# Performance work log

Hardware: AMD Instinct MI355X
Metric: run time of the kernel (lower is better)

Reference implementation:

```python
import jax, jax.numpy as jnp
import numpy as np

B, L, D = 2, 2048, 2048
H, HKV, HD = 32, 8, 64
G = H // HKV  # GQA group size


def _rope(t, cos, sin):
    # t: [B, h, L, HD]; cos/sin: [L, HD//2]; pairs are consecutive (view_as_complex)
    tr, ti = t[..., 0::2], t[..., 1::2]
    out_r = tr * cos - ti * sin
    out_i = tr * sin + ti * cos
    return jnp.stack([out_r, out_i], axis=-1).reshape(t.shape)


def setup_inputs() -> dict:
    key = jax.random.key(0)
    ks = jax.random.split(key, 5)
    x = jax.random.normal(ks[0], (B, L, D), dtype=jnp.float32)
    wq = jax.random.normal(ks[1], (D, H * HD), dtype=jnp.float32) * 0.02
    wk = jax.random.normal(ks[2], (D, HKV * HD), dtype=jnp.float32) * 0.02
    wv = jax.random.normal(ks[3], (D, HKV * HD), dtype=jnp.float32) * 0.02
    wo = jax.random.normal(ks[4], (D, D), dtype=jnp.float32) * 0.02
    # RoPE freqs: theta_i = 10000^(-2i/HD), angle[p, i] = p * theta_i
    inv_freq = 1.0 / (10000.0 ** (jnp.arange(0, HD, 2, dtype=jnp.float32) / HD))
    angles = jnp.arange(L, dtype=jnp.float32)[:, None] * inv_freq[None, :]  # [L, HD//2]
    freqs_cos = jnp.cos(angles)
    freqs_sin = jnp.sin(angles)
    # additive causal mask [L, L]
    mask = jnp.where(jnp.tril(jnp.ones((L, L), dtype=bool)), 0.0, -1e9).astype(jnp.float32)
    return {"x": x, "wq": wq, "wk": wk, "wv": wv, "wo": wo,
            "freqs_cos": freqs_cos, "freqs_sin": freqs_sin, "mask": mask}


def reference(x, wq, wk, wv, wo, freqs_cos, freqs_sin, mask):
    b, l, _ = x.shape
    q = (x @ wq).reshape(b, l, H, HD).transpose(0, 2, 1, 3)      # [B, H, L, HD]
    k = (x @ wk).reshape(b, l, HKV, HD).transpose(0, 2, 1, 3)    # [B, HKV, L, HD]
    v = (x @ wv).reshape(b, l, HKV, HD).transpose(0, 2, 1, 3)
    q = _rope(q, freqs_cos, freqs_sin)
    k = _rope(k, freqs_cos, freqs_sin)
    # native GQA broadcast instead of repeat_kv copy (same math)
    qg = q.reshape(b, HKV, G, l, HD)
    scores = jnp.einsum("bhgqd,bhkd->bhgqk", qg, k) / jnp.sqrt(jnp.float32(HD))
    scores = scores + mask  # [B, HKV, G, L, L]
    probs = jax.nn.softmax(scores.astype(jnp.float32), axis=-1).astype(v.dtype)
    out = jnp.einsum("bhgqk,bhkd->bhgqd", probs, v)              # [B, HKV, G, L, HD]
    out = out.reshape(b, H, l, HD).transpose(0, 2, 1, 3).reshape(b, l, H * HD)
    return out @ wo
```

## Files before the change

### kernel.cpp

```cpp
#include <hip/hip_runtime.h>
#include <hip/hip_bf16.h>

#define B_   2
#define L_   2048
#define D_   2048
#define H_   32
#define HKV_ 8
#define HD_  64
#define G_   4
#define M_   4096
#define NF_  3072

typedef __attribute__((ext_vector_type(8))) short bf16x8;
typedef __attribute__((ext_vector_type(4))) float f32x4;

static __device__ __forceinline__ unsigned short f2bf(float f) {
  unsigned int u = __float_as_uint(f);
  unsigned int r = (u + 0x7FFFu + ((u >> 16) & 1u)) >> 16;
  return (unsigned short)r;
}

#define GLD16(g, l) __builtin_amdgcn_global_load_lds(                      \
    (const __attribute__((address_space(1))) void*)(g),                    \
    (__attribute__((address_space(3))) void*)(l), 16, 0, 0)

__global__ void cast_bf16_kernel(const float* __restrict__ in,
                                 unsigned short* __restrict__ out, int n4) {
  int i = blockIdx.x * blockDim.x + threadIdx.x;
  if (i >= n4) return;
  float4 v = ((const float4*)in)[i];
  uint2 r;
  r.x = (unsigned int)f2bf(v.x) | ((unsigned int)f2bf(v.y) << 16);
  r.y = (unsigned int)f2bf(v.z) | ((unsigned int)f2bf(v.w) << 16);
  ((uint2*)out)[i] = r;
}

__global__ void transpose_cast_kernel(const float* __restrict__ src,
                                      unsigned short* __restrict__ dst,
                                      int K, int N) {
  __shared__ float tile[32][33];
  int k0 = blockIdx.y * 32, n0 = blockIdx.x * 32;
  int tx = threadIdx.x, ty = threadIdx.y;
#pragma unroll
  for (int r = 0; r < 4; ++r)
    tile[ty * 4 + r][tx] = src[(size_t)(k0 + ty * 4 + r) * N + n0 + tx];
  __syncthreads();
#pragma unroll
  for (int r = 0; r < 4; ++r)
    dst[(size_t)(n0 + ty * 4 + r) * K + k0 + tx] = f2bf(tile[tx][ty * 4 + r]);
}

__global__ __launch_bounds__(256)
void gemm_bt_kernel(const unsigned short* __restrict__ A,
                    const unsigned short* __restrict__ Bt,
                    float* __restrict__ C, int M, int N, int K) {
  __shared__ unsigned short Al[128 * 32];
  __shared__ unsigned short Bl[128 * 32];
  const int tid = threadIdx.x;
  const int w = tid >> 6;
  const int l = tid & 63;
  const int row0 = blockIdx.y * 128;
  const int col0 = blockIdx.x * 128;
  const int wr = (w >> 1) * 64, wc = (w & 1) * 64;

  f32x4 acc[4][4];
#pragma unroll
  for (int m = 0; m < 4; ++m)
#pragma unroll
    for (int n = 0; n < 4; ++n) acc[m][n] = (f32x4){0.f, 0.f, 0.f, 0.f};

  const int srow = l >> 2;
  const int scol = (l & 3) * 8;
  const int fr = l & 15, fk = (l >> 4) * 8;
  const int nk = K / 32;

  for (int kt = 0; kt < nk; ++kt) {
    const int k0 = kt * 32;
#pragma unroll
    for (int t = 0; t < 2; ++t) {
      const int rr = (w * 2 + t) * 16 + srow;
      GLD16(A + (size_t)(row0 + rr) * K + k0 + scol, &Al[(w * 2 + t) * 512]);
      GLD16(Bt + (size_t)(col0 + rr) * K + k0 + scol, &Bl[(w * 2 + t) * 512]);
    }
    __syncthreads();
    bf16x8 af[4], bfr[4];
#pragma unroll
    for (int m = 0; m < 4; ++m)
      af[m] = *(const bf16x8*)&Al[(wr + m * 16 + fr) * 32 + fk];
#pragma unroll
    for (int n = 0; n < 4; ++n)
      bfr[n] = *(const bf16x8*)&Bl[(wc + n * 16 + fr) * 32 + fk];
#pragma unroll
    for (int m = 0; m < 4; ++m)
#pragma unroll
      for (int n = 0; n < 4; ++n)
        acc[m][n] = __builtin_amdgcn_mfma_f32_16x16x32_bf16(af[m], bfr[n], acc[m][n], 0, 0, 0);
    __syncthreads();
  }

  const int fq = l >> 4;
#pragma unroll
  for (int m = 0; m < 4; ++m)
#pragma unroll
    for (int n = 0; n < 4; ++n)
#pragma unroll
      for (int j = 0; j < 4; ++j) {
        int r = row0 + wr + m * 16 + fq * 4 + j;
        int c = col0 + wc + n * 16 + fr;
        C[(size_t)r * N + c] = acc[m][n][j];
      }
}

__global__ void rope_kernel(const float* __restrict__ src,
                            const float* __restrict__ cosf,
                            const float* __restrict__ sinf,
                            unsigned short* __restrict__ dst, int nh, int col_off,
                            int total) {
  int idx = blockIdx.x * blockDim.x + threadIdx.x;
  if (idx >= total) return;
  int i = idx & 31;
  int h = (idx >> 5) & (nh - 1);
  int row = idx / (nh << 5);
  int lpos = row & (L_ - 1);
  int b = row >> 11;
  const float* s = src + (size_t)row * NF_ + col_off + h * 64 + 2 * i;
  float tr = s[0], ti = s[1];
  float c = cosf[lpos * 32 + i], sn = sinf[lpos * 32 + i];
  float orr = tr * c - ti * sn;
  float oii = tr * sn + ti * c;
  size_t o = (((size_t)(b * nh + h)) * L_ + lpos) * 64 + 2 * i;
  unsigned int packed = (unsigned int)f2bf(orr) | ((unsigned int)f2bf(oii) << 16);
  *(unsigned int*)&dst[o] = packed;
}

__global__ void cast_vT_kernel(const float* __restrict__ v,
                               unsigned short* __restrict__ vT) {
  __shared__ float tile[32][33];
  int l0 = blockIdx.x * 32, d0 = blockIdx.y * 32;
  int z = blockIdx.z;
  int b = z >> 3, hkv = z & 7;
  int tx = threadIdx.x, ty = threadIdx.y;
  const float* src = v + (size_t)(b * L_) * NF_ + 2560 + hkv * 64;
#pragma unroll
  for (int r = 0; r < 4; ++r)
    tile[ty * 4 + r][tx] = src[(size_t)(l0 + ty * 4 + r) * NF_ + d0 + tx];
  __syncthreads();
  unsigned short* dst = vT + ((size_t)z * 64) * L_;
#pragma unroll
  for (int r = 0; r < 4; ++r)
    dst[(size_t)(d0 + ty * 4 + r) * L_ + l0 + tx] = f2bf(tile[tx][ty * 4 + r]);
}

__global__ __launch_bounds__(256)
void attn_kernel(const unsigned short* __restrict__ Q,
                 const unsigned short* __restrict__ Kt,
                 const unsigned short* __restrict__ Vt,
                 unsigned short* __restrict__ O) {
  __shared__ unsigned short Kl[64 * 64];
  __shared__ unsigned short Vl[64 * 64];
  __shared__ unsigned short Pl[64 * 64];
  const int tid = threadIdx.x, w = tid >> 6, l = tid & 63;
  const int bh = blockIdx.x;
  const int b = bh >> 5, h = bh & 31;
  const int hkv = h >> 2;
  const int by = blockIdx.y;
  const int q0 = by * 128;
  const int fr = l & 15, hi = l >> 4;
  const int frx = fr & 7;

  const int srow = l >> 3;
  const int scole = ((l & 7) ^ srow) * 8;

  const unsigned short* kbase = Kt + ((size_t)(b * HKV_ + hkv)) * L_ * 64;
  const unsigned short* vbase = Vt + ((size_t)(b * HKV_ + hkv)) * 64 * L_;

  bf16x8 qf[2][2];
#pragma unroll
  for (int s = 0; s < 2; ++s) {
    const unsigned short* qb =
        Q + (((size_t)bh) * L_ + q0 + s * 64 + w * 16 + fr) * 64 + hi * 8;
    qf[s][0] = *(const bf16x8*)(qb);
    qf[s][1] = *(const bf16x8*)(qb + 32);
  }

  float m_i[2][4], l_i[2][4];
  f32x4 oacc[2][4];
#pragma unroll
  for (int s = 0; s < 2; ++s)
#pragma unroll
    for (int j = 0; j < 4; ++j) { m_i[s][j] = -1e30f; l_i[s][j] = 0.f; }
#pragma unroll
  for (int s = 0; s < 2; ++s)
#pragma unroll
    for (int nf = 0; nf < 4; ++nf) oacc[s][nf] = (f32x4){0.f, 0.f, 0.f, 0.f};

  const int nt = 2 * by + 2;

  for (int t = 0; t < nt; ++t) {
    const int kv0 = t * 64;
#pragma unroll
    for (int u = 0; u < 2; ++u) {
      const int c = w * 2 + u;
      const int rr = c * 8 + srow;
      GLD16(kbase + ((size_t)(kv0 + rr)) * 64 + scole, &Kl[c * 512]);
      GLD16(vbase + ((size_t)rr) * L_ + kv0 + scole, &Vl[c * 512]);
    }
    __syncthreads();

#pragma unroll
    for (int s = 0; s < 2; ++s) {
      if (t > 2 * by + s) continue;

      f32x4 sacc[4];
#pragma unroll
      for (int nf = 0; nf < 4; ++nf) sacc[nf] = (f32x4){0.f, 0.f, 0.f, 0.f};
#pragma unroll
      for (int ks = 0; ks < 2; ++ks) {
#pragma unroll
        for (int nf = 0; nf < 4; ++nf) {
          bf16x8 kfrag = *(const bf16x8*)
              &Kl[(nf * 16 + fr) * 64 + (((ks * 4 + hi) ^ frx) * 8)];
          sacc[nf] = __builtin_amdgcn_mfma_f32_16x16x32_bf16(qf[s][ks], kfrag, sacc[nf], 0, 0, 0);
        }
      }

      const int rbase = q0 + s * 64 + w * 16 + hi * 4;
      float sv[4][4];
#pragma unroll
      for (int nf = 0; nf < 4; ++nf)
#pragma unroll
        for (int j = 0; j < 4; ++j) {
          float sval = sacc[nf][j] * 0.125f;
          if (kv0 + nf * 16 + fr > rbase + j) sval = -1e30f;
          sv[nf][j] = sval;
        }
#pragma unroll
      for (int j = 0; j < 4; ++j) {
        float mx = fmaxf(fmaxf(sv[0][j], sv[1][j]), fmaxf(sv[2][j], sv[3][j]));
        mx = fmaxf(mx, __shfl_xor(mx, 1));
        mx = fmaxf(mx, __shfl_xor(mx, 2));
        mx = fmaxf(mx, __shfl_xor(mx, 4));
        mx = fmaxf(mx, __shfl_xor(mx, 8));
        float mnew = fmaxf(m_i[s][j], mx);
        float cr = __expf(m_i[s][j] - mnew);
        m_i[s][j] = mnew;
        float psum = 0.f;
#pragma unroll
        for (int nf = 0; nf < 4; ++nf) {
          float pp = __expf(sv[nf][j] - mnew);
          sv[nf][j] = pp;
          psum += pp;
        }
        psum += __shfl_xor(psum, 1);
        psum += __shfl_xor(psum, 2);
        psum += __shfl_xor(psum, 4);
        psum += __shfl_xor(psum, 8);
        l_i[s][j] = l_i[s][j] * cr + psum;
#pragma unroll
        for (int nf = 0; nf < 4; ++nf) oacc[s][nf][j] *= cr;
        const int prow = w * 16 + hi * 4 + j;
#pragma unroll
        for (int nf = 0; nf < 4; ++nf)
          Pl[prow * 64 + (((nf * 2 + (fr >> 3)) ^ (prow & 7)) * 8) + frx] =
              f2bf(sv[nf][j]);
      }

#pragma unroll
      for (int ks = 0; ks < 2; ++ks) {
        bf16x8 pa = *(const bf16x8*)
            &Pl[(w * 16 + fr) * 64 + (((ks * 4 + hi) ^ frx) * 8)];
#pragma unroll
        for (int nf = 0; nf < 4; ++nf) {
          bf16x8 vfrag = *(const bf16x8*)
              &Vl[(nf * 16 + fr) * 64 + (((ks * 4 + hi) ^ frx) * 8)];
          oacc[s][nf] = __builtin_amdgcn_mfma_f32_16x16x32_bf16(pa, vfrag, oacc[s][nf], 0, 0, 0);
        }
      }
    }
    __syncthreads();
  }

#pragma unroll
  for (int s = 0; s < 2; ++s)
#pragma unroll
    for (int nf = 0; nf < 4; ++nf)
#pragma unroll
      for (int j = 0; j < 4; ++j) {
        int qrow = q0 + s * 64 + w * 16 + hi * 4 + j;
        int d = nf * 16 + fr;
        float val = oacc[s][nf][j] / l_i[s][j];
        O[((size_t)(b * L_ + qrow)) * 2048 + h * 64 + d] = f2bf(val);
      }
}

extern "C" void kernel_launch(void* const* d_in, const int* in_sizes, int n_in,
                              void* d_out, int out_size, void* d_ws, size_t ws_size,
                              hipStream_t stream) {
  (void)in_sizes; (void)n_in; (void)out_size; (void)ws_size;
  const float* x  = (const float*)d_in[0];
  const float* wq = (const float*)d_in[1];
  const float* wk = (const float*)d_in[2];
  const float* wv = (const float*)d_in[3];
  const float* wo = (const float*)d_in[4];
  const float* fc = (const float*)d_in[5];
  const float* fs = (const float*)d_in[6];
  float* out = (float*)d_out;

  char* ws = (char*)d_ws;
  unsigned short* x_b  = (unsigned short*)(ws + 0);
  unsigned short* wT   = (unsigned short*)(ws + 16777216);
  unsigned short* woT  = (unsigned short*)(ws + 29360128);
  float* qkv_f         = (float*)(ws + 37748736);
  unsigned short* at_b = (unsigned short*)(ws + 37748736);
  unsigned short* q_b  = (unsigned short*)(ws + 88080384);
  unsigned short* k_b  = (unsigned short*)(ws + 104857600);
  unsigned short* vT_b = (unsigned short*)(ws + 109051904);

  dim3 tb(32, 8);
  cast_bf16_kernel<<<8192, 256, 0, stream>>>(x, x_b, M_ * D_ / 4);
  transpose_cast_kernel<<<dim3(64, 64), tb, 0, stream>>>(wq, wT, 2048, 2048);
  transpose_cast_kernel<<<dim3(16, 64), tb, 0, stream>>>(wk, wT + (size_t)2048 * 2048, 2048, 512);
  transpose_cast_kernel<<<dim3(16, 64), tb, 0, stream>>>(wv, wT + (size_t)2560 * 2048, 2048, 512);
  transpose_cast_kernel<<<dim3(64, 64), tb, 0, stream>>>(wo, woT, 2048, 2048);

  gemm_bt_kernel<<<dim3(24, 32), 256, 0, stream>>>(x_b, wT, qkv_f, M_, NF_, 2048);

  rope_kernel<<<16384, 256, 0, stream>>>(qkv_f, fc, fs, q_b, 32, 0, M_ * 32 * 32);
  rope_kernel<<<4096, 256, 0, stream>>>(qkv_f, fc, fs, k_b, 8, 2048, M_ * 8 * 32);
  cast_vT_kernel<<<dim3(64, 2, 16), tb, 0, stream>>>(qkv_f, vT_b);

  attn_kernel<<<dim3(64, 16), 256, 0, stream>>>(q_b, k_b, vT_b, at_b);

  gemm_bt_kernel<<<dim3(16, 32), 256, 0, stream>>>(at_b, woT, out, M_, 2048, 2048);
}
```

Baseline: 445.8 us.

## Balance causal attention blocks, fold softmax scale into Q, lazy rescaling

Each attention block now handles two query tiles paired from opposite ends of the causal triangle (by and 15-by), which halves the grid and gives every block the same amount of work. The 1/sqrt(d)·log2(e) factor is folded into Q during RoPE so the kernel can use exp2 without a per-score multiply. The causal mask is applied only on the diagonal tile. Online-softmax rescaling is skipped unless some row's max grows by more than 8, and the row-sum reduction is deferred to the end. Hardware bf16 conversion replaces the manual rounding, and the larger per-block work reduces block-level parallelism to 512 blocks.

```diff
diff --git a/kernel.cpp b/kernel.cpp
--- a/kernel.cpp
+++ b/kernel.cpp
@@ -18,6 +18,10 @@
   unsigned int u = __float_as_uint(f);
   unsigned int r = (u + 0x7FFFu + ((u >> 16) & 1u)) >> 16;
   return (unsigned short)r;
+}
+static __device__ __forceinline__ unsigned short f2bf_hw(float f) {
+  __hip_bfloat16 h = __float2bfloat16(f);
+  return *(unsigned short*)&h;
 }
 
 #define GLD16(g, l) __builtin_amdgcn_global_load_lds(                      \
@@ -115,7 +119,7 @@
                             const float* __restrict__ cosf,
                             const float* __restrict__ sinf,
                             unsigned short* __restrict__ dst, int nh, int col_off,
-                            int total) {
+                            float scale, int total) {
   int idx = blockIdx.x * blockDim.x + threadIdx.x;
   if (idx >= total) return;
   int i = idx & 31;
@@ -126,8 +130,8 @@
   const float* s = src + (size_t)row * NF_ + col_off + h * 64 + 2 * i;
   float tr = s[0], ti = s[1];
   float c = cosf[lpos * 32 + i], sn = sinf[lpos * 32 + i];
-  float orr = tr * c - ti * sn;
-  float oii = tr * sn + ti * c;
+  float orr = (tr * c - ti * sn) * scale;
+  float oii = (tr * sn + ti * c) * scale;
   size_t o = (((size_t)(b * nh + h)) * L_ + lpos) * 64 + 2 * i;
   unsigned int packed = (unsigned int)f2bf(orr) | ((unsigned int)f2bf(oii) << 16);
   *(unsigned int*)&dst[o] = packed;
@@ -163,8 +167,7 @@
   const int bh = blockIdx.x;
   const int b = bh >> 5, h = bh & 31;
   const int hkv = h >> 2;
-  const int by = blockIdx.y;
-  const int q0 = by * 128;
+  const int pair = blockIdx.y;
   const int fr = l & 15, hi = l >> 4;
   const int frx = fr & 7;
 
@@ -174,123 +177,144 @@
   const unsigned short* kbase = Kt + ((size_t)(b * HKV_ + hkv)) * L_ * 64;
   const unsigned short* vbase = Vt + ((size_t)(b * HKV_ + hkv)) * 64 * L_;
 
-  bf16x8 qf[2][2];
-#pragma unroll
-  for (int s = 0; s < 2; ++s) {
-    const unsigned short* qb =
-        Q + (((size_t)bh) * L_ + q0 + s * 64 + w * 16 + fr) * 64 + hi * 8;
-    qf[s][0] = *(const bf16x8*)(qb);
-    qf[s][1] = *(const bf16x8*)(qb + 32);
+  for (int half = 0; half < 2; ++half) {
+    const int by = half ? (15 - pair) : pair;
+    const int q0 = by * 128;
+
+    bf16x8 qf[2][2];
+#pragma unroll
+    for (int s = 0; s < 2; ++s) {
+      const unsigned short* qb =
+          Q + (((size_t)bh) * L_ + q0 + s * 64 + w * 16 + fr) * 64 + hi * 8;
+      qf[s][0] = *(const bf16x8*)(qb);
+      qf[s][1] = *(const bf16x8*)(qb + 32);
+    }
+
+    float m_i[2][4], l_p[2][4];
+    f32x4 oacc[2][4];
+#pragma unroll
+    for (int s = 0; s < 2; ++s)
+#pragma unroll
+      for (int j = 0; j < 4; ++j) { m_i[s][j] = -1e30f; l_p[s][j] = 0.f; }
+#pragma unroll
+    for (int s = 0; s < 2; ++s)
+#pragma unroll
+      for (int nf = 0; nf < 4; ++nf) oacc[s][nf] = (f32x4){0.f, 0.f, 0.f, 0.f};
+
+    const int nt = 2 * by + 2;
+
+    for (int t = 0; t < nt; ++t) {
+      const int kv0 = t * 64;
+#pragma unroll
+      for (int u = 0; u < 2; ++u) {
+        const int c = w * 2 + u;
+        const int rr = c * 8 + srow;
+        GLD16(kbase + ((size_t)(kv0 + rr)) * 64 + scole, &Kl[c * 512]);
+        GLD16(vbase + ((size_t)rr) * L_ + kv0 + scole, &Vl[c * 512]);
+      }
+      __syncthreads();
+
+#pragma unroll
+      for (int s = 0; s < 2; ++s) {
+        const int dlim = 2 * by + s;
+        if (t > dlim) continue;
+
+        f32x4 sacc[4];
+#pragma unroll
+        for (int nf = 0; nf < 4; ++nf) sacc[nf] = (f32x4){0.f, 0.f, 0.f, 0.f};
+#pragma unroll
+        for (int ks = 0; ks < 2; ++ks) {
+#pragma unroll
+          for (int nf = 0; nf < 4; ++nf) {
+            bf16x8 kfrag = *(const bf16x8*)
+                &Kl[(nf * 16 + fr) * 64 + (((ks * 4 + hi) ^ frx) * 8)];
+            sacc[nf] = __builtin_amdgcn_mfma_f32_16x16x32_bf16(qf[s][ks], kfrag, sacc[nf], 0, 0, 0);
+          }
+        }
+
+        if (t == dlim) {
+          const int rbase = q0 + s * 64 + w * 16 + hi * 4;
+#pragma unroll
+          for (int nf = 0; nf < 4; ++nf)
+#pragma unroll
+            for (int j = 0; j < 4; ++j)
+              if (kv0 + nf * 16 + fr > rbase + j) sacc[nf][j] = -1e30f;
+        }
+
+        float rowmax[4];
+#pragma unroll
+        for (int j = 0; j < 4; ++j) {
+          float mx = fmaxf(fmaxf(sacc[0][j], sacc[1][j]),
+                           fmaxf(sacc[2][j], sacc[3][j]));
+          mx = fmaxf(mx, __shfl_xor(mx, 1));
+          mx = fmaxf(mx, __shfl_xor(mx, 2));
+          mx = fmaxf(mx, __shfl_xor(mx, 4));
+          mx = fmaxf(mx, __shfl_xor(mx, 8));
+          rowmax[j] = mx;
+        }
+
+        float g = rowmax[0] - m_i[s][0];
+        g = fmaxf(g, rowmax[1] - m_i[s][1]);
+        g = fmaxf(g, rowmax[2] - m_i[s][2]);
+        g = fmaxf(g, rowmax[3] - m_i[s][3]);
+        if (!__all(g <= 8.f)) {
+#pragma unroll
+          for (int j = 0; j < 4; ++j) {
+            float mnew = fmaxf(m_i[s][j], rowmax[j]);
+            float cr = exp2f(m_i[s][j] - mnew);
+            m_i[s][j] = mnew;
+            l_p[s][j] *= cr;
+#pragma unroll
+            for (int nf = 0; nf < 4; ++nf) oacc[s][nf][j] *= cr;
+          }
+        }
+
+#pragma unroll
+        for (int j = 0; j < 4; ++j) {
+          const int prow = w * 16 + hi * 4 + j;
+#pragma unroll
+          for (int nf = 0; nf < 4; ++nf) {
+            float p = exp2f(sacc[nf][j] - m_i[s][j]);
+            l_p[s][j] += p;
+            Pl[prow * 64 + (((nf * 2 + (fr >> 3)) ^ (prow & 7)) * 8) + frx] =
+                f2bf_hw(p);
+          }
+        }
+
+#pragma unroll
+        for (int ks = 0; ks < 2; ++ks) {
+          bf16x8 pa = *(const bf16x8*)
+              &Pl[(w * 16 + fr) * 64 + (((ks * 4 + hi) ^ frx) * 8)];
+#pragma unroll
+          for (int nf = 0; nf < 4; ++nf) {
+            bf16x8 vfrag = *(const bf16x8*)
+                &Vl[(nf * 16 + fr) * 64 + (((ks * 4 + hi) ^ frx) * 8)];
+            oacc[s][nf] = __builtin_amdgcn_mfma_f32_16x16x32_bf16(pa, vfrag, oacc[s][nf], 0, 0, 0);
+          }
+        }
+      }
+      __syncthreads();
+    }
+
+#pragma unroll
+    for (int s = 0; s < 2; ++s)
+#pragma unroll
+      for (int j = 0; j < 4; ++j) {
+        float lsum = l_p[s][j];
+        lsum += __shfl_xor(lsum, 1);
+        lsum += __shfl_xor(lsum, 2);
+        lsum += __shfl_xor(lsum, 4);
+        lsum += __shfl_xor(lsum, 8);
+        float inv = 1.0f / lsum;
+#pragma unroll
+        for (int nf = 0; nf < 4; ++nf) {
+          int qrow = q0 + s * 64 + w * 16 + hi * 4 + j;
+          int d = nf * 16 + fr;
+          O[((size_t)(b * L_ + qrow)) * 2048 + h * 64 + d] =
+              f2bf_hw(oacc[s][nf][j] * inv);
+        }
+      }
   }
-
-  float m_i[2][4], l_i[2][4];
-  f32x4 oacc[2][4];
-#pragma unroll
-  for (int s = 0; s < 2; ++s)
-#pragma unroll
-    for (int j = 0; j < 4; ++j) { m_i[s][j] = -1e30f; l_i[s][j] = 0.f; }
-#pragma unroll
-  for (int s = 0; s < 2; ++s)
-#pragma unroll
-    for (int nf = 0; nf < 4; ++nf) oacc[s][nf] = (f32x4){0.f, 0.f, 0.f, 0.f};
-
-  const int nt = 2 * by + 2;
-
-  for (int t = 0; t < nt; ++t) {
-    const int kv0 = t * 64;
-#pragma unroll
-    for (int u = 0; u < 2; ++u) {
-      const int c = w * 2 + u;
-      const int rr = c * 8 + srow;
-      GLD16(kbase + ((size_t)(kv0 + rr)) * 64 + scole, &Kl[c * 512]);
-      GLD16(vbase + ((size_t)rr) * L_ + kv0 + scole, &Vl[c * 512]);
-    }
-    __syncthreads();
-
-#pragma unroll
-    for (int s = 0; s < 2; ++s) {
-      if (t > 2 * by + s) continue;
-
-      f32x4 sacc[4];
-#pragma unroll
-      for (int nf = 0; nf < 4; ++nf) sacc[nf] = (f32x4){0.f, 0.f, 0.f, 0.f};
-#pragma unroll
-      for (int ks = 0; ks < 2; ++ks) {
-#pragma unroll
-        for (int nf = 0; nf < 4; ++nf) {
-          bf16x8 kfrag = *(const bf16x8*)
-              &Kl[(nf * 16 + fr) * 64 + (((ks * 4 + hi) ^ frx) * 8)];
-          sacc[nf] = __builtin_amdgcn_mfma_f32_16x16x32_bf16(qf[s][ks], kfrag, sacc[nf], 0, 0, 0);
-        }
-      }
-
-      const int rbase = q0 + s * 64 + w * 16 + hi * 4;
-      float sv[4][4];
-#pragma unroll
-      for (int nf = 0; nf < 4; ++nf)
-#pragma unroll
-        for (int j = 0; j < 4; ++j) {
-          float sval = sacc[nf][j] * 0.125f;
-          if (kv0 + nf * 16 + fr > rbase + j) sval = -1e30f;
-          sv[nf][j] = sval;
-        }
-#pragma unroll
-      for (int j = 0; j < 4; ++j) {
-        float mx = fmaxf(fmaxf(sv[0][j], sv[1][j]), fmaxf(sv[2][j], sv[3][j]));
-        mx = fmaxf(mx, __shfl_xor(mx, 1));
-        mx = fmaxf(mx, __shfl_xor(mx, 2));
-        mx = fmaxf(mx, __shfl_xor(mx, 4));
-        mx = fmaxf(mx, __shfl_xor(mx, 8));
-        float mnew = fmaxf(m_i[s][j], mx);
-        float cr = __expf(m_i[s][j] - mnew);
-        m_i[s][j] = mnew;
-        float psum = 0.f;
-#pragma unroll
-        for (int nf = 0; nf < 4; ++nf) {
-          float pp = __expf(sv[nf][j] - mnew);
-          sv[nf][j] = pp;
-          psum += pp;
-        }
-        psum += __shfl_xor(psum, 1);
-        psum += __shfl_xor(psum, 2);
-        psum += __shfl_xor(psum, 4);
-        psum += __shfl_xor(psum, 8);
-        l_i[s][j] = l_i[s][j] * cr + psum;
-#pragma unroll
-        for (int nf = 0; nf < 4; ++nf) oacc[s][nf][j] *= cr;
-        const int prow = w * 16 + hi * 4 + j;
-#pragma unroll
-        for (int nf = 0; nf < 4; ++nf)
-          Pl[prow * 64 + (((nf * 2 + (fr >> 3)) ^ (prow & 7)) * 8) + frx] =
-              f2bf(sv[nf][j]);
-      }
-
-#pragma unroll
-      for (int ks = 0; ks < 2; ++ks) {
-        bf16x8 pa = *(const bf16x8*)
-            &Pl[(w * 16 + fr) * 64 + (((ks * 4 + hi) ^ frx) * 8)];
-#pragma unroll
-        for (int nf = 0; nf < 4; ++nf) {
-          bf16x8 vfrag = *(const bf16x8*)
-              &Vl[(nf * 16 + fr) * 64 + (((ks * 4 + hi) ^ frx) * 8)];
-          oacc[s][nf] = __builtin_amdgcn_mfma_f32_16x16x32_bf16(pa, vfrag, oacc[s][nf], 0, 0, 0);
-        }
-      }
-    }
-    __syncthreads();
-  }
-
-#pragma unroll
-  for (int s = 0; s < 2; ++s)
-#pragma unroll
-    for (int nf = 0; nf < 4; ++nf)
-#pragma unroll
-      for (int j = 0; j < 4; ++j) {
-        int qrow = q0 + s * 64 + w * 16 + hi * 4 + j;
-        int d = nf * 16 + fr;
-        float val = oacc[s][nf][j] / l_i[s][j];
-        O[((size_t)(b * L_ + qrow)) * 2048 + h * 64 + d] = f2bf(val);
-      }
 }
 
 extern "C" void kernel_launch(void* const* d_in, const int* in_sizes, int n_in,
@@ -316,6 +340,8 @@
   unsigned short* k_b  = (unsigned short*)(ws + 104857600);
   unsigned short* vT_b = (unsigned short*)(ws + 109051904);
 
+  const float qscale = 0.125f * 1.4426950408889634f;
+
   dim3 tb(32, 8);
   cast_bf16_kernel<<<8192, 256, 0, stream>>>(x, x_b, M_ * D_ / 4);
   transpose_cast_kernel<<<dim3(64, 64), tb, 0, stream>>>(wq, wT, 2048, 2048);
@@ -325,11 +351,11 @@
 
   gemm_bt_kernel<<<dim3(24, 32), 256, 0, stream>>>(x_b, wT, qkv_f, M_, NF_, 2048);
 
-  rope_kernel<<<16384, 256, 0, stream>>>(qkv_f, fc, fs, q_b, 32, 0, M_ * 32 * 32);
-  rope_kernel<<<4096, 256, 0, stream>>>(qkv_f, fc, fs, k_b, 8, 2048, M_ * 8 * 32);
+  rope_kernel<<<16384, 256, 0, stream>>>(qkv_f, fc, fs, q_b, 32, 0, qscale, M_ * 32 * 32);
+  rope_kernel<<<4096, 256, 0, stream>>>(qkv_f, fc, fs, k_b, 8, 2048, 1.0f, M_ * 8 * 32);
   cast_vT_kernel<<<dim3(64, 2, 16), tb, 0, stream>>>(qkv_f, vT_b);
 
-  attn_kernel<<<dim3(64, 16), 256, 0, stream>>>(q_b, k_b, vT_b, at_b);
+  attn_kernel<<<dim3(64, 8), 256, 0, stream>>>(q_b, k_b, vT_b, at_b);
 
   gemm_bt_kernel<<<dim3(16, 32), 256, 0, stream>>>(at_b, woT, out, M_, 2048, 2048);
 }
```

Result: faster. 399.0 us (-10.5%).
